# Kernel optimization log

Measured on AMD Instinct MI355X. Metric: run time of the kernel, lower is better.

The kernel has to match this reference:

```python
import jax, jax.numpy as jnp
import numpy as np

N_NODES = 10000
N_EDGES = 640000
D = 128            # node_dims == edge_dims
HID = 2 * D        # ff hidden
EPS = 1e-6


def _layernorm(x, g, b):
    mu = jnp.mean(x, axis=-1, keepdims=True)
    var = jnp.var(x, axis=-1, keepdims=True)
    return (x - mu) * jax.lax.rsqrt(var + EPS) * g + b


def setup_inputs() -> dict:
    key = jax.random.key(0)
    ks = jax.random.split(key, 16)
    def lin(k, fan_in, fan_out):
        lim = 1.0 / np.sqrt(fan_in)
        kw, kb = jax.random.split(k)
        W = jax.random.uniform(kw, (fan_in, fan_out), jnp.float32, -lim, lim)
        b = jax.random.uniform(kb, (fan_out,), jnp.float32, -lim, lim)
        return W, b
    x = jax.random.normal(ks[0], (N_NODES, D), jnp.float32)
    edge_index = jax.random.randint(ks[1], (2, N_EDGES), 0, N_NODES, jnp.int64)
    edge_attr = jax.random.normal(ks[2], (N_EDGES, D), jnp.float32)
    # message MLP: Linear(3D->D), ReLU, Linear(D->D), ReLU, Linear(D->D)
    W1, b1 = lin(ks[3], 3 * D, D)
    W2, b2 = lin(ks[4], D, D)
    W3, b3 = lin(ks[5], D, D)
    # feedforward: Linear(D->2D), ReLU, Linear(2D->D)
    F1, bf1 = lin(ks[6], D, HID)
    F2, bf2 = lin(ks[7], HID, D)
    g0 = jnp.ones((D,), jnp.float32); be0 = jnp.zeros((D,), jnp.float32)
    g1 = jnp.ones((D,), jnp.float32); be1 = jnp.zeros((D,), jnp.float32)
    return {"x": x, "edge_index": edge_index, "edge_attr": edge_attr,
            "W1": W1, "b1": b1, "W2": W2, "b2": b2, "W3": W3, "b3": b3,
            "F1": F1, "bf1": bf1, "F2": F2, "bf2": bf2,
            "g0": g0, "be0": be0, "g1": g1, "be1": be1}


def reference(x, edge_index, edge_attr, W1, b1, W2, b2, W3, b3,
              F1, bf1, F2, bf2, g0, be0, g1, be1):
    src = edge_index[0]  # j
    dst = edge_index[1]  # i
    # message: cat([h_V_i, edge_attr, h_V_j]) -> MLP  (E x 3D gather)
    m = jnp.concatenate([x[dst], edge_attr, x[src]], axis=-1)
    m = jax.nn.relu(m @ W1 + b1)
    m = jax.nn.relu(m @ W2 + b2)
    m = m @ W3 + b3  # [E, D]
    # scatter-mean over destination nodes
    sums = jax.ops.segment_sum(m, dst, num_segments=N_NODES)
    cnt = jax.ops.segment_sum(jnp.ones((N_EDGES,), m.dtype), dst, num_segments=N_NODES)
    dh = sums / jnp.maximum(cnt, 1.0)[:, None]
    # residual + norm (dropout is identity at inference)
    h = _layernorm(x + dh, g0, be0)
    # pointwise feedforward
    ff = jax.nn.relu(h @ F1 + bf1) @ F2 + bf2
    return _layernorm(h + ff, g1, be1)
```

## Files before the change

### kernel.cpp

```cpp
#include <hip/hip_runtime.h>


#define NE 640000
#define NN 10000
#define DD 128
#define HIDN 256
#define EPSF 1e-6f

typedef __attribute__((ext_vector_type(8))) short short8;
typedef __attribute__((ext_vector_type(4))) float f32x4;

__device__ __forceinline__ unsigned short f2bf(float f) {
    union { float f; unsigned int u; } v; v.f = f;
    unsigned int r = v.u + 0x7FFFu + ((v.u >> 16) & 1u);
    return (unsigned short)(r >> 16);
}
__device__ __forceinline__ float bf2f(unsigned short h) {
    union { unsigned int u; float f; } v; v.u = ((unsigned int)h) << 16;
    return v.f;
}

__global__ void prep_hist(const float* __restrict__ W1,
                          const float* __restrict__ W2,
                          const float* __restrict__ W3,
                          unsigned short* __restrict__ WT,
                          const int* __restrict__ ei,
                          int* __restrict__ cursor)
{
    int e = blockIdx.x * 256 + threadIdx.x;
    if (e < NE) atomicAdd(cursor + ei[(long)NE + e], 1);
    if (blockIdx.x < 192) {
        int g = blockIdx.x * 256 + threadIdx.x;
        int layer = g >> 14, r = g & 16383;
        int n = r >> 7, k = r & 127;
        const float* W = (layer == 0) ? (W1 + 128 * DD) : (layer == 1 ? W2 : W3);
        WT[layer * 16384 + n * 128 + ((((k >> 3) ^ (n & 7)) << 3) | (k & 7))] =
            f2bf(W[k * DD + n]);
    }
}

__global__ __launch_bounds__(256, 2)
void pq_kernel(const float* __restrict__ x, const float* __restrict__ W1,
               const float* __restrict__ b1,
               unsigned short* __restrict__ Pb, unsigned short* __restrict__ Qb)
{
    __shared__ float sXT[128 * 68];
    __shared__ float sB[32 * 128];
    const int t = threadIdx.x;
    const int nb = blockIdx.x * 64;
    const int r0 = (t >> 4) << 2, c0 = (t & 15) << 3;

#pragma unroll
    for (int p = 0; p < 8; ++p) {
        int f = t + p * 256;
        int row = f >> 5, c4 = (f & 31) << 2;
        int node = nb + row; if (node >= NN) node = NN - 1;
        float4 v = *(const float4*)(x + (long)node * DD + c4);
        sXT[(c4 + 0) * 68 + row] = v.x;
        sXT[(c4 + 1) * 68 + row] = v.y;
        sXT[(c4 + 2) * 68 + row] = v.z;
        sXT[(c4 + 3) * 68 + row] = v.w;
    }

    for (int pass = 0; pass < 2; ++pass) {
        const float* W = W1 + (pass == 0 ? 0 : 256 * DD);
        float acc[4][8];
#pragma unroll
        for (int i = 0; i < 4; ++i)
#pragma unroll
            for (int j = 0; j < 8; ++j) acc[i][j] = 0.f;

        for (int kc = 0; kc < 4; ++kc) {
            __syncthreads();
#pragma unroll
            for (int p = 0; p < 4; ++p) {
                int f = t + p * 256;
                int kr = f >> 5, col = (f & 31) << 2;
                *(float4*)(sB + kr * 128 + col) =
                    *(const float4*)(W + (long)(kc * 32 + kr) * DD + col);
            }
            __syncthreads();
#pragma unroll 4
            for (int k = 0; k < 32; ++k) {
                float4 a  = *(const float4*)(sXT + (kc * 32 + k) * 68 + r0);
                float4 bl = *(const float4*)(sB + k * 128 + c0);
                float4 bh = *(const float4*)(sB + k * 128 + c0 + 4);
                float av[4] = {a.x, a.y, a.z, a.w};
                float bv[8] = {bl.x, bl.y, bl.z, bl.w, bh.x, bh.y, bh.z, bh.w};
#pragma unroll
                for (int i = 0; i < 4; ++i)
#pragma unroll
                    for (int j = 0; j < 8; ++j)
                        acc[i][j] = fmaf(av[i], bv[j], acc[i][j]);
            }
        }
        unsigned short* Out = (pass == 0) ? Pb : Qb;
#pragma unroll
        for (int i = 0; i < 4; ++i) {
            int node = nb + r0 + i;
            if (node < NN) {
                unsigned short tmp[8];
#pragma unroll
                for (int j = 0; j < 8; ++j) {
                    float v = acc[i][j] + (pass == 0 ? b1[c0 + j] : 0.f);
                    tmp[j] = f2bf(v);
                }
                *(uint4*)(Out + (long)node * 128 + c0) = *(uint4*)tmp;
            }
        }
    }
}

__global__ __launch_bounds__(1024)
void scan_kernel(int* __restrict__ cursor, float* __restrict__ cnt)
{
    __shared__ int sp[1024];
    const int t = threadIdx.x;
    const int base = t * 10;
    int v[10], loc[10];
    int s = 0;
#pragma unroll
    for (int i = 0; i < 10; ++i) {
        int n = base + i;
        v[i] = (n < NN) ? cursor[n] : 0;
        loc[i] = s; s += v[i];
    }
    sp[t] = s;
    __syncthreads();
    for (int off = 1; off < 1024; off <<= 1) {
        int x = 0;
        if (t >= off) x = sp[t - off];
        __syncthreads();
        sp[t] += x;
        __syncthreads();
    }
    int excl = sp[t] - s;
#pragma unroll
    for (int i = 0; i < 10; ++i) {
        int n = base + i;
        if (n < NN) {
            cursor[n] = excl + loc[i];
            cnt[n] = (float)v[i];
        }
    }
}

__global__ void scatter_kernel(const int* __restrict__ ei,
                               int* __restrict__ cursor, int* __restrict__ perm)
{
    int e = blockIdx.x * 256 + threadIdx.x;
    if (e < NE) {
        int d = ei[(long)NE + e];
        int p = atomicAdd(cursor + d, 1);
        perm[p] = e;
    }
}

__device__ __forceinline__ const short8* frag(const unsigned short* buf,
                                              int row, int kc, int q)
{
    int g = (kc * 4 + q) ^ (row & 7);
    return (const short8*)(buf + row * 128 + g * 8);
}

__global__ __launch_bounds__(256, 2)
void edge_mfma(const float* __restrict__ ea, const int* __restrict__ ei,
               const int* __restrict__ perm,
               const unsigned short* __restrict__ WT,
               const unsigned short* __restrict__ Pb,
               const unsigned short* __restrict__ Qb,
               const float* __restrict__ b2, const float* __restrict__ b3,
               float* __restrict__ sums)
{
    __shared__ __align__(16) char smem[1536 + 64 * 132 * 4];
    int*            sE   = (int*)smem;
    int*            sDst = (int*)(smem + 512);
    int*            sSrc = (int*)(smem + 1024);
    unsigned short* sA = (unsigned short*)(smem + 1536);
    float*          sM = (float*)(smem + 1536);

    const int t = threadIdx.x;
    const int wave = t >> 6, lane = t & 63;
    const int ln = lane & 15, q = lane >> 4;
    const int r0 = wave * 32;
    const long pbase = (long)blockIdx.x * 128;

    if (t < 128) {
        int e = perm[pbase + t];
        sE[t] = e;
        sDst[t] = ei[(long)NE + e];
        sSrc[t] = ei[e];
    }
    __syncthreads();

#pragma unroll
    for (int p = 0; p < 16; ++p) {
        int f = t + p * 256;
        int row = f >> 5, c4 = (f & 31) << 2;
        float4 v = *(const float4*)(ea + (long)sE[row] * DD + c4);
        uint2 pk;
        pk.x = (unsigned)f2bf(v.x) | ((unsigned)f2bf(v.y) << 16);
        pk.y = (unsigned)f2bf(v.z) | ((unsigned)f2bf(v.w) << 16);
        int addr = row * 128 + ((((c4 >> 3) ^ (row & 7)) << 3) | (c4 & 7));
        *(uint2*)(sA + addr) = pk;
    }
    __syncthreads();

    f32x4 acc[2][8];

#pragma unroll
    for (int rt = 0; rt < 2; ++rt)
#pragma unroll
        for (int ct = 0; ct < 8; ++ct) acc[rt][ct] = (f32x4)(0.f);
#pragma unroll
    for (int kc = 0; kc < 4; ++kc) {
        short8 a0 = *frag(sA, r0 + ln,      kc, q);
        short8 a1 = *frag(sA, r0 + 16 + ln, kc, q);
#pragma unroll
        for (int ct = 0; ct < 8; ++ct) {
            short8 b = *frag(WT, ct * 16 + ln, kc, q);
            acc[0][ct] = __builtin_amdgcn_mfma_f32_16x16x32_bf16(a0, b, acc[0][ct], 0, 0, 0);
            acc[1][ct] = __builtin_amdgcn_mfma_f32_16x16x32_bf16(a1, b, acc[1][ct], 0, 0, 0);
        }
    }
    __syncthreads();

#pragma unroll
    for (int p = 0; p < 8; ++p) {
        int f = t + p * 256;
        int row = f >> 4, g = f & 15;
        uint4 v = *(const uint4*)(Qb + (long)sSrc[row] * DD + g * 8);
        *(uint4*)(sA + row * 128 + ((g ^ (row & 7)) << 3)) = v;
    }
    __syncthreads();

#pragma unroll
    for (int rt = 0; rt < 2; ++rt)
#pragma unroll
        for (int rg = 0; rg < 4; ++rg) {
            int row = r0 + rt * 16 + q * 4 + rg;
            long dof = (long)sDst[row] * DD;
#pragma unroll
            for (int ct = 0; ct < 8; ++ct) {
                int col = ct * 16 + ln;
                int slot = row * 128 + ((((col >> 3) ^ (row & 7)) << 3) | (col & 7));
                float v = acc[rt][ct][rg] + bf2f(Pb[dof + col]) + bf2f(sA[slot]);
                sA[slot] = f2bf(fmaxf(v, 0.f));
            }
        }

#pragma unroll
    for (int rt = 0; rt < 2; ++rt)
#pragma unroll
        for (int ct = 0; ct < 8; ++ct) acc[rt][ct] = (f32x4)(0.f);
#pragma unroll
    for (int kc = 0; kc < 4; ++kc) {
        short8 a0 = *frag(sA, r0 + ln,      kc, q);
        short8 a1 = *frag(sA, r0 + 16 + ln, kc, q);
#pragma unroll
        for (int ct = 0; ct < 8; ++ct) {
            short8 b = *frag(WT + 16384, ct * 16 + ln, kc, q);
            acc[0][ct] = __builtin_amdgcn_mfma_f32_16x16x32_bf16(a0, b, acc[0][ct], 0, 0, 0);
            acc[1][ct] = __builtin_amdgcn_mfma_f32_16x16x32_bf16(a1, b, acc[1][ct], 0, 0, 0);
        }
    }
    float bv2[8];
#pragma unroll
    for (int ct = 0; ct < 8; ++ct) bv2[ct] = b2[ct * 16 + ln];
#pragma unroll
    for (int rt = 0; rt < 2; ++rt)
#pragma unroll
        for (int rg = 0; rg < 4; ++rg) {
            int row = r0 + rt * 16 + q * 4 + rg;
#pragma unroll
            for (int ct = 0; ct < 8; ++ct) {
                int col = ct * 16 + ln;
                int slot = row * 128 + ((((col >> 3) ^ (row & 7)) << 3) | (col & 7));
                sA[slot] = f2bf(fmaxf(acc[rt][ct][rg] + bv2[ct], 0.f));
            }
        }

#pragma unroll
    for (int rt = 0; rt < 2; ++rt)
#pragma unroll
        for (int ct = 0; ct < 8; ++ct) acc[rt][ct] = (f32x4)(0.f);
#pragma unroll
    for (int kc = 0; kc < 4; ++kc) {
        short8 a0 = *frag(sA, r0 + ln,      kc, q);
        short8 a1 = *frag(sA, r0 + 16 + ln, kc, q);
#pragma unroll
        for (int ct = 0; ct < 8; ++ct) {
            short8 b = *frag(WT + 2 * 16384, ct * 16 + ln, kc, q);
            acc[0][ct] = __builtin_amdgcn_mfma_f32_16x16x32_bf16(a0, b, acc[0][ct], 0, 0, 0);
            acc[1][ct] = __builtin_amdgcn_mfma_f32_16x16x32_bf16(a1, b, acc[1][ct], 0, 0, 0);
        }
    }
    __syncthreads();

    float bv3[8];
#pragma unroll
    for (int ct = 0; ct < 8; ++ct) bv3[ct] = b3[ct * 16 + ln];

    if (wave < 2) {
#pragma unroll
        for (int rt = 0; rt < 2; ++rt)
#pragma unroll
            for (int rg = 0; rg < 4; ++rg) {
                int row = r0 + rt * 16 + q * 4 + rg;
#pragma unroll
                for (int ct = 0; ct < 8; ++ct)
                    sM[row * 132 + ct * 16 + ln] = acc[rt][ct][rg] + bv3[ct];
            }
    }
    __syncthreads();
    {
        const int c = t & 127, h = t >> 7;
        const int rb = h * 32;
        float a = 0.f;
        int cur = sDst[rb];
#pragma unroll 8
        for (int r = rb; r < rb + 32; ++r) {
            int d = sDst[r];
            if (d != cur) {
                atomicAdd(sums + (long)cur * DD + c, a);
                a = 0.f; cur = d;
            }
            a += sM[r * 132 + c];
        }
        atomicAdd(sums + (long)cur * DD + c, a);
    }
    __syncthreads();
    if (wave >= 2) {
#pragma unroll
        for (int rt = 0; rt < 2; ++rt)
#pragma unroll
            for (int rg = 0; rg < 4; ++rg) {
                int row = r0 + rt * 16 + q * 4 + rg;
#pragma unroll
                for (int ct = 0; ct < 8; ++ct)
                    sM[(row - 64) * 132 + ct * 16 + ln] = acc[rt][ct][rg] + bv3[ct];
            }
    }
    __syncthreads();
    {
        const int c = t & 127, h = t >> 7;
        const int rb = h * 32;
        float a = 0.f;
        int cur = sDst[64 + rb];
#pragma unroll 8
        for (int r = rb; r < rb + 32; ++r) {
            int d = sDst[64 + r];
            if (d != cur) {
                atomicAdd(sums + (long)cur * DD + c, a);
                a = 0.f; cur = d;
            }
            a += sM[r * 132 + c];
        }
        atomicAdd(sums + (long)cur * DD + c, a);
    }
}

__global__ __launch_bounds__(256)
void node_fused(const float* __restrict__ x,
                const float* __restrict__ sums, const float* __restrict__ cnt,
                const float* __restrict__ F1, const float* __restrict__ bf1,
                const float* __restrict__ F2, const float* __restrict__ bf2,
                const float* __restrict__ g0, const float* __restrict__ be0,
                const float* __restrict__ g1, const float* __restrict__ be1,
                float* __restrict__ out)
{
    constexpr int NPB = 8;
    __shared__ float sh[NPB][DD];
    __shared__ float shid[NPB][HIDN];
    __shared__ float sz[NPB][DD];

    const int t = threadIdx.x;
    const int wave = t >> 6, lane = t & 63;
    const int half = lane >> 5, l2 = lane & 31;
    const int nl = wave * 2 + half;
    const int node = blockIdx.x * NPB + nl;
    const long base = (long)node * DD;

    float inv = 1.0f / fmaxf(cnt[node], 1.0f);
    float y[4], s = 0.f, ss = 0.f;
#pragma unroll
    for (int e = 0; e < 4; ++e) {
        int c = l2 + 32 * e;
        y[e] = x[base + c] + sums[base + c] * inv;
        s += y[e]; ss += y[e] * y[e];
    }
#pragma unroll
    for (int off = 16; off > 0; off >>= 1) {
        s += __shfl_down(s, off, 32); ss += __shfl_down(ss, off, 32);
    }
    s = __shfl(s, 0, 32); ss = __shfl(ss, 0, 32);
    float mean = s * (1.0f / DD);
    float var  = ss * (1.0f / DD) - mean * mean;
    float rstd = rsqrtf(var + EPSF);
#pragma unroll
    for (int e = 0; e < 4; ++e) {
        int c = l2 + 32 * e;
        sh[nl][c] = (y[e] - mean) * rstd * g0[c] + be0[c];
    }
    __syncthreads();

    float hacc[NPB];
    float bb = bf1[t];
#pragma unroll
    for (int v = 0; v < NPB; ++v) hacc[v] = bb;
    for (int k = 0; k < DD; ++k) {
        float wv = F1[(long)k * HIDN + t];
#pragma unroll
        for (int v = 0; v < NPB; ++v) hacc[v] = fmaf(sh[v][k], wv, hacc[v]);
    }
#pragma unroll
    for (int v = 0; v < NPB; ++v) shid[v][t] = fmaxf(hacc[v], 0.f);
    __syncthreads();

    const int col = t & (DD - 1);
    const int grp = (t >> 7) * 4;
    float o[4];
#pragma unroll
    for (int v = 0; v < 4; ++v) o[v] = bf2[col];
    for (int k = 0; k < HIDN; ++k) {
        float wv = F2[(long)k * DD + col];
#pragma unroll
        for (int v = 0; v < 4; ++v) o[v] = fmaf(shid[grp + v][k], wv, o[v]);
    }
#pragma unroll
    for (int v = 0; v < 4; ++v) sz[grp + v][col] = sh[grp + v][col] + o[v];
    __syncthreads();

    float z[4]; s = 0.f; ss = 0.f;
#pragma unroll
    for (int e = 0; e < 4; ++e) {
        int c = l2 + 32 * e;
        z[e] = sz[nl][c]; s += z[e]; ss += z[e] * z[e];
    }
#pragma unroll
    for (int off = 16; off > 0; off >>= 1) {
        s += __shfl_down(s, off, 32); ss += __shfl_down(ss, off, 32);
    }
    s = __shfl(s, 0, 32); ss = __shfl(ss, 0, 32);
    mean = s * (1.0f / DD);
    var  = ss * (1.0f / DD) - mean * mean;
    rstd = rsqrtf(var + EPSF);
#pragma unroll
    for (int e = 0; e < 4; ++e) {
        int c = l2 + 32 * e;
        out[base + c] = (z[e] - mean) * rstd * g1[c] + be1[c];
    }
}

extern "C" void kernel_launch(void* const* d_in, const int* in_sizes, int n_in,
                              void* d_out, int out_size, void* d_ws, size_t ws_size,
                              hipStream_t stream)
{
    const float* x   = (const float*)d_in[0];
    const int*   ei  = (const int*)  d_in[1];
    const float* ea  = (const float*)d_in[2];
    const float* W1  = (const float*)d_in[3];
    const float* b1  = (const float*)d_in[4];
    const float* W2  = (const float*)d_in[5];
    const float* b2  = (const float*)d_in[6];
    const float* W3  = (const float*)d_in[7];
    const float* b3  = (const float*)d_in[8];
    const float* F1  = (const float*)d_in[9];
    const float* bf1 = (const float*)d_in[10];
    const float* F2  = (const float*)d_in[11];
    const float* bf2 = (const float*)d_in[12];
    const float* g0  = (const float*)d_in[13];
    const float* be0 = (const float*)d_in[14];
    const float* g1  = (const float*)d_in[15];
    const float* be1 = (const float*)d_in[16];
    float* out = (float*)d_out;

    char* ws = (char*)d_ws;
    float*          sums   = (float*)(ws);
    float*          cnt    = (float*)(ws + 5120000);
    unsigned short* WT     = (unsigned short*)(ws + 5160192);
    unsigned short* Pb     = (unsigned short*)(ws + 5258752);
    unsigned short* Qb     = (unsigned short*)(ws + 7818752);
    int*            cursor = (int*)(ws + 10378752);
    int*            perm   = (int*)(ws + 10418752);

    hipMemsetAsync(ws, 0, 5120000, stream);
    hipMemsetAsync(ws + 10378752, 0, 40000, stream);
    prep_hist<<<NE / 256, 256, 0, stream>>>(W1, W2, W3, WT, ei, cursor);
    pq_kernel<<<(NN + 63) / 64, 256, 0, stream>>>(x, W1, b1, Pb, Qb);
    scan_kernel<<<1, 1024, 0, stream>>>(cursor, cnt);
    scatter_kernel<<<NE / 256, 256, 0, stream>>>(ei, cursor, perm);
    edge_mfma<<<NE / 128, 256, 0, stream>>>(ea, ei, perm, WT, Pb, Qb,
                                            b2, b3, sums);
    node_fused<<<NN / 8, 256, 0, stream>>>(x, sums, cnt, F1, bf1, F2, bf2,
                                           g0, be0, g1, be1, out);
}
```

Before: 861.3 us.

## Stage edge MLP weight tiles in LDS and cache destination indices

The edge kernel now copies each 128x128 bf16 weight matrix into a shared-memory buffer before its MFMA stage, so B fragments are read from LDS instead of from global memory through cache. Destination indices are also loaded into registers once, and the node feed-forward loops get an unroll-8 pragma. In exchange, shared memory per block rises to about 67KB, adding two barriers and extra copy traffic per block, and the larger LDS footprint may limit how many blocks fit per CU.

```diff
diff --git a/kernel.cpp b/kernel.cpp
--- a/kernel.cpp
+++ b/kernel.cpp
@@ -172,11 +172,12 @@
                const float* __restrict__ b2, const float* __restrict__ b3,
                float* __restrict__ sums)
 {
-    __shared__ __align__(16) char smem[1536 + 64 * 132 * 4];
+    __shared__ __align__(16) char smem[1536 + 65536];
     int*            sE   = (int*)smem;
     int*            sDst = (int*)(smem + 512);
     int*            sSrc = (int*)(smem + 1024);
     unsigned short* sA = (unsigned short*)(smem + 1536);
+    unsigned short* sW = (unsigned short*)(smem + 1536 + 32768);
     float*          sM = (float*)(smem + 1536);
 
     const int t = threadIdx.x;
@@ -191,7 +192,20 @@
         sDst[t] = ei[(long)NE + e];
         sSrc[t] = ei[e];
     }
-    __syncthreads();
+    {
+        const uint4* src = (const uint4*)WT;
+        uint4* dst = (uint4*)sW;
+#pragma unroll
+        for (int p = 0; p < 8; ++p) dst[t + p * 256] = src[t + p * 256];
+    }
+    __syncthreads();
+
+    int drow[8];
+#pragma unroll
+    for (int rt = 0; rt < 2; ++rt)
+#pragma unroll
+        for (int rg = 0; rg < 4; ++rg)
+            drow[rt * 4 + rg] = sDst[r0 + rt * 16 + q * 4 + rg];
 
 #pragma unroll
     for (int p = 0; p < 16; ++p) {
@@ -218,13 +232,19 @@
         short8 a1 = *frag(sA, r0 + 16 + ln, kc, q);
 #pragma unroll
         for (int ct = 0; ct < 8; ++ct) {
-            short8 b = *frag(WT, ct * 16 + ln, kc, q);
+            short8 b = *frag(sW, ct * 16 + ln, kc, q);
             acc[0][ct] = __builtin_amdgcn_mfma_f32_16x16x32_bf16(a0, b, acc[0][ct], 0, 0, 0);
             acc[1][ct] = __builtin_amdgcn_mfma_f32_16x16x32_bf16(a1, b, acc[1][ct], 0, 0, 0);
         }
     }
     __syncthreads();
 
+    {
+        const uint4* src = (const uint4*)(WT + 16384);
+        uint4* dst = (uint4*)sW;
+#pragma unroll
+        for (int p = 0; p < 8; ++p) dst[t + p * 256] = src[t + p * 256];
+    }
 #pragma unroll
     for (int p = 0; p < 8; ++p) {
         int f = t + p * 256;
@@ -239,7 +259,7 @@
 #pragma unroll
         for (int rg = 0; rg < 4; ++rg) {
             int row = r0 + rt * 16 + q * 4 + rg;
-            long dof = (long)sDst[row] * DD;
+            long dof = (long)drow[rt * 4 + rg] * DD;
 #pragma unroll
             for (int ct = 0; ct < 8; ++ct) {
                 int col = ct * 16 + ln;
@@ -259,10 +279,18 @@
         short8 a1 = *frag(sA, r0 + 16 + ln, kc, q);
 #pragma unroll
         for (int ct = 0; ct < 8; ++ct) {
-            short8 b = *frag(WT + 16384, ct * 16 + ln, kc, q);
+            short8 b = *frag(sW, ct * 16 + ln, kc, q);
             acc[0][ct] = __builtin_amdgcn_mfma_f32_16x16x32_bf16(a0, b, acc[0][ct], 0, 0, 0);
             acc[1][ct] = __builtin_amdgcn_mfma_f32_16x16x32_bf16(a1, b, acc[1][ct], 0, 0, 0);
         }
+    }
+    __syncthreads();
+
+    {
+        const uint4* src = (const uint4*)(WT + 2 * 16384);
+        uint4* dst = (uint4*)sW;
+#pragma unroll
+        for (int p = 0; p < 8; ++p) dst[t + p * 256] = src[t + p * 256];
     }
     float bv2[8];
 #pragma unroll
@@ -279,6 +307,7 @@
                 sA[slot] = f2bf(fmaxf(acc[rt][ct][rg] + bv2[ct], 0.f));
             }
         }
+    __syncthreads();
 
 #pragma unroll
     for (int rt = 0; rt < 2; ++rt)
@@ -290,7 +319,7 @@
         short8 a1 = *frag(sA, r0 + 16 + ln, kc, q);
 #pragma unroll
         for (int ct = 0; ct < 8; ++ct) {
-            short8 b = *frag(WT + 2 * 16384, ct * 16 + ln, kc, q);
+            short8 b = *frag(sW, ct * 16 + ln, kc, q);
             acc[0][ct] = __builtin_amdgcn_mfma_f32_16x16x32_bf16(a0, b, acc[0][ct], 0, 0, 0);
             acc[1][ct] = __builtin_amdgcn_mfma_f32_16x16x32_bf16(a1, b, acc[1][ct], 0, 0, 0);
         }
@@ -408,6 +437,7 @@
     float bb = bf1[t];
 #pragma unroll
     for (int v = 0; v < NPB; ++v) hacc[v] = bb;
+#pragma unroll 8
     for (int k = 0; k < DD; ++k) {
         float wv = F1[(long)k * HIDN + t];
 #pragma unroll
@@ -422,6 +452,7 @@
     float o[4];
 #pragma unroll
     for (int v = 0; v < 4; ++v) o[v] = bf2[col];
+#pragma unroll 8
     for (int k = 0; k < HIDN; ++k) {
         float wv = F2[(long)k * DD + col];
 #pragma unroll
```

Result: faster. 781.6 us (-9.3%).
